# Kernel tuning notes

Measured on AMD Instinct MI355X. Metric: run time of the kernel, lower is better.

Reference implementation:

```python
import jax, jax.numpy as jnp
import numpy as np

NUM_EMBEDDINGS = 4096
EMBEDDING_DIM = 512
N_TOKENS = 32768
COMMITMENT_COST = 0.25


def setup_inputs() -> dict:
    key = jax.random.key(0)
    k1, k2 = jax.random.split(key)
    flat_input = jax.random.normal(k1, (N_TOKENS, EMBEDDING_DIM), dtype=jnp.float32)
    # torch init: uniform(-1/K, 1/K)
    weight = jax.random.uniform(k2, (NUM_EMBEDDINGS, EMBEDDING_DIM), dtype=jnp.float32,
                                minval=-1.0 / NUM_EMBEDDINGS, maxval=1.0 / NUM_EMBEDDINGS)
    return {"flat_input": flat_input, "weight": weight}


def reference(flat_input, weight):
    distances = (jnp.sum(flat_input ** 2, axis=1, keepdims=True)
                 + jnp.sum(weight ** 2, axis=1)
                 - 2.0 * jnp.matmul(flat_input, weight.T))
    encoding_indices = jnp.argmin(distances, axis=1)  # [N]
    # one-hot @ weight == direct gather of codebook rows
    quantized = weight[encoding_indices]  # [N, D]

    e_latent_loss = jnp.mean((jax.lax.stop_gradient(quantized) - flat_input) ** 2, axis=1)
    q_latent_loss = jnp.mean((quantized - jax.lax.stop_gradient(flat_input)) ** 2, axis=1)
    loss = q_latent_loss + COMMITMENT_COST * e_latent_loss  # [N]

    # straight-through estimator
    quantized_st = flat_input + jax.lax.stop_gradient(quantized - flat_input)

    # avg_probs = mean of one-hot encodings over batch = normalized code counts
    counts = jnp.zeros((NUM_EMBEDDINGS,), dtype=flat_input.dtype).at[encoding_indices].add(1.0)
    avg_probs = counts / flat_input.shape[0]
    perplexity = jnp.exp(-jnp.sum(avg_probs * jnp.log(avg_probs + 1e-10)))

    return quantized_st, loss, perplexity, encoding_indices
```

## Files before the change

kernel.cpp:

```cpp
#include <hip/hip_runtime.h>
#include <math.h>

#define N_TOK 32768
#define K_CODES 4096
#define DIM 512
#define COMMIT 0.25f
#define NCAND 8
#define NSPLIT 2
#define SPLIT_CODES (K_CODES / NSPLIT)
#define NITER (SPLIT_CODES / 256)
#define BIAS 0.125f

typedef short s16x8 __attribute__((ext_vector_type(8)));
typedef float f32x4 __attribute__((ext_vector_type(4)));
typedef unsigned int uint32;
typedef unsigned long long u64;
typedef unsigned short u16;

__device__ __forceinline__ u16 f2bf(float f) {
    uint32 b = __float_as_uint(f);
    return (u16)((b + 0x7FFFu + ((b >> 16) & 1u)) >> 16);
}

__device__ __forceinline__ void gload16(const u16* g, u16* l) {
    __builtin_amdgcn_global_load_lds(
        (const __attribute__((address_space(1))) void*)g,
        (__attribute__((address_space(3))) void*)l,
        16, 0, 0);
}

__global__ __launch_bounds__(256) void tobf16_kernel(const float* __restrict__ src,
                                                     u16* __restrict__ dst, int n4) {
    int i = blockIdx.x * 256 + threadIdx.x;
    int stride = gridDim.x * 256;
    for (; i < n4; i += stride) {
        float4 v = ((const float4*)src)[i];
        ushort4 o;
        o.x = f2bf(v.x); o.y = f2bf(v.y); o.z = f2bf(v.z); o.w = f2bf(v.w);
        ((ushort4*)dst)[i] = o;
    }
}

__global__ __launch_bounds__(256) void rowsq_np_kernel(const float* __restrict__ a,
                                                       float* __restrict__ out,
                                                       int nrows) {
    #pragma clang fp contract(off)
    const int gw   = (blockIdx.x * 256 + threadIdx.x) >> 6;
    const int lane = threadIdx.x & 63;
    const int row  = gw * 8 + (lane >> 3);
    const int j    = lane & 7;
    if (row >= nrows) return;
    const float* p = a + (size_t)row * DIM;
    float blk[4];
    #pragma unroll
    for (int b = 0; b < 4; ++b) {
        const float* q = p + b * 128;
        float v = q[j];
        float r = v * v;
        for (int i = 8; i < 128; i += 8) { float u = q[i + j]; r += u * u; }
        float s1 = r  + __shfl_xor(r, 1);
        float s2 = s1 + __shfl_xor(s1, 2);
        float s3 = s2 + __shfl_xor(s2, 4);
        blk[b] = s3;
    }
    float res = (blk[0] + blk[1]) + (blk[2] + blk[3]);
    if (j == 0) out[row] = res;
}

__global__ __launch_bounds__(512, 2) void screen_kernel(const u16* __restrict__ xb,
                                                        const u16* __restrict__ wb,
                                                        const float* __restrict__ w2f,
                                                        u64* __restrict__ candPart) {
    __shared__ __attribute__((aligned(16))) u16 POOL[49152];

    const int tid  = threadIdx.x;
    const int wv   = tid >> 6;
    const int wt   = wv >> 2;
    const int wc   = wv & 3;
    const int lane = tid & 63;
    const int quad = lane >> 4;
    const int n15  = lane & 15;
    const int m0   = blockIdx.x * 128;
    const int sbase = blockIdx.y * SPLIT_CODES;

    const int l8  = lane >> 3;
    const int qsw = (lane & 7) ^ l8;

    const u16* xg0 = xb + (size_t)(m0 + wv * 16 + 0 + l8) * DIM + qsw * 8;
    const u16* xg1 = xb + (size_t)(m0 + wv * 16 + 8 + l8) * DIM + qsw * 8;
    const size_t wofs0 = (size_t)(wv * 32 + 0  + l8) * DIM;
    const size_t wofs1 = (size_t)(wv * 32 + 8  + l8) * DIM;
    const size_t wofs2 = (size_t)(wv * 32 + 16 + l8) * DIM;
    const size_t wofs3 = (size_t)(wv * 32 + 24 + l8) * DIM;

    u16* ldsx0 = &POOL[0     + wv * 1024];
    u16* ldsx1 = &POOL[8192  + wv * 1024];
    u16* ldsw0 = &POOL[16384 + wv * 2048];
    u16* ldsw1 = &POOL[32768 + wv * 2048];

    uint32 r1[16], r2[16];
    #pragma unroll
    for (int i = 0; i < 16; ++i) { r1[i] = 0xFFFFFFFFu; r2[i] = 0xFFFFFFFFu; }

    const u16* wit = wb + (size_t)sbase * DIM + qsw * 8;

    {
        gload16(xg0, ldsx0);
        gload16(xg0 + 512, ldsx0 + 512);
    }
    gload16(xg1, ldsx0 + 512);
    gload16(wit + wofs0, ldsw0);
    gload16(wit + wofs1, ldsw0 + 512);
    gload16(wit + wofs2, ldsw0 + 1024);
    gload16(wit + wofs3, ldsw0 + 1536);
    __syncthreads();

    for (int it = 0; it < NITER; ++it) {
        const int nbase = sbase + it * 256;

        float w2pb[4];
        #pragma unroll
        for (int c = 0; c < 4; ++c) w2pb[c] = w2f[nbase + wc * 64 + c * 16 + n15] + BIAS;

        f32x4 acc[4][4];
        #pragma unroll
        for (int i = 0; i < 4; ++i)
            #pragma unroll
            for (int c = 0; c < 4; ++c) acc[i][c] = (f32x4){0.f, 0.f, 0.f, 0.f};

        for (int kc = 0; kc < 8; ++kc) {
            if (kc < 7) {
                const int nb = (kc + 1) & 1;
                u16* lx = nb ? ldsx1 : ldsx0;
                u16* lw = nb ? ldsw1 : ldsw0;
                const int ko = (kc + 1) * 64;
                gload16(xg0 + ko, lx);
                gload16(xg1 + ko, lx + 512);
                gload16(wit + wofs0 + ko, lw);
                gload16(wit + wofs1 + ko, lw + 512);
                gload16(wit + wofs2 + ko, lw + 1024);
                gload16(wit + wofs3 + ko, lw + 1536);
            } else if (it < NITER - 1) {
                const u16* wn = wit + (size_t)256 * DIM;
                gload16(xg0, ldsx0);
                gload16(xg1, ldsx0 + 512);
                gload16(wn + wofs0, ldsw0);
                gload16(wn + wofs1, ldsw0 + 512);
                gload16(wn + wofs2, ldsw0 + 1024);
                gload16(wn + wofs3, ldsw0 + 1536);
            }

            const u16* X = &POOL[(kc & 1) * 8192];
            const u16* W = &POOL[16384 + (kc & 1) * 16384];
            #pragma unroll
            for (int s = 0; s < 2; ++s) {
                const int lq = s * 4 + quad;
                s16x8 af[4], bf[4];
                #pragma unroll
                for (int i = 0; i < 4; ++i) {
                    const int tr = wt * 64 + i * 16 + n15;
                    af[i] = *(const s16x8*)&X[tr * 64 + (lq ^ (tr & 7)) * 8];
                }
                #pragma unroll
                for (int c = 0; c < 4; ++c) {
                    const int cr = wc * 64 + c * 16 + n15;
                    bf[c] = *(const s16x8*)&W[cr * 64 + (lq ^ (cr & 7)) * 8];
                }
                #pragma unroll
                for (int i = 0; i < 4; ++i)
                    #pragma unroll
                    for (int c = 0; c < 4; ++c)
                        acc[i][c] = __builtin_amdgcn_mfma_f32_16x16x32_bf16(af[i], bf[c], acc[i][c], 0, 0, 0);
            }
            __syncthreads();
        }

        #pragma unroll
        for (int i = 0; i < 4; ++i)
            #pragma unroll
            for (int r = 0; r < 4; ++r) {
                const int ti = i * 4 + r;
                #pragma unroll
                for (int c = 0; c < 4; ++c) {
                    float s = fmaf(-2.0f, acc[i][c][r], w2pb[c]);
                    uint32 key = (__float_as_uint(s) & 0xFFFFFFC0u) | (uint32)((it << 2) | c);
                    uint32 mx = r1[ti] > key ? r1[ti] : key;
                    r1[ti] = r1[ti] < key ? r1[ti] : key;
                    r2[ti] = r2[ti] < mx ? r2[ti] : mx;
                }
            }
        wit += (size_t)256 * DIM;
    }

    u64* MS = (u64*)POOL;
    for (int phase = 0; phase < 2; ++phase) {
        __syncthreads();
        if (wt == phase) {
            #pragma unroll
            for (int ti = 0; ti < 16; ++ti) {
                const int i = ti >> 2, r = ti & 3;
                const int tloc = i * 16 + quad * 4 + r;
                #pragma unroll
                for (int e = 0; e < 2; ++e) {
                    uint32 k  = e ? r2[ti] : r1[ti];
                    uint32 vb = k & 0xFFFFFFC0u;
                    uint32 id = k & 63u;
                    uint32 code = (uint32)(sbase + (id >> 2) * 256 + wc * 64 + (id & 3) * 16 + n15);
                    MS[tloc * 128 + (wc * 16 + n15) * 2 + e] = ((u64)vb << 32) | code;
                }
            }
        }
        __syncthreads();
        if (tid < 64) {
            u64 best[6];
            #pragma unroll
            for (int c = 0; c < 6; ++c) best[c] = 0xFFFFFFFFFFFFFFFFull;
            for (int e = 0; e < 128; ++e) {
                u64 v = MS[tid * 128 + e];
                if (v < best[5]) {
                    best[5] = v;
                    #pragma unroll
                    for (int p = 5; p > 0; --p)
                        if (best[p] < best[p - 1]) { u64 tv = best[p]; best[p] = best[p - 1]; best[p - 1] = tv; }
                }
            }
            const int token = m0 + phase * 64 + tid;
            u64* dst = candPart + ((size_t)blockIdx.y * N_TOK + token) * 6;
            #pragma unroll
            for (int c = 0; c < 6; ++c) dst[c] = best[c];
        }
    }
}

__global__ __launch_bounds__(256) void mergecand_kernel(const u64* __restrict__ candPart,
                                                        int* __restrict__ candF) {
    int t = blockIdx.x * 256 + threadIdx.x;
    u64 best[NCAND];
    #pragma unroll
    for (int c = 0; c < NCAND; ++c) best[c] = 0xFFFFFFFFFFFFFFFFull;
    for (int s = 0; s < NSPLIT; ++s) {
        const u64* src = candPart + ((size_t)s * N_TOK + t) * 6;
        #pragma unroll
        for (int c = 0; c < 6; ++c) {
            u64 v = src[c];
            if (v < best[NCAND - 1]) {
                best[NCAND - 1] = v;
                #pragma unroll
                for (int p = NCAND - 1; p > 0; --p)
                    if (best[p] < best[p - 1]) { u64 tv = best[p]; best[p] = best[p - 1]; best[p - 1] = tv; }
            }
        }
    }
    #pragma unroll
    for (int c = 0; c < NCAND; ++c) candF[(size_t)t * NCAND + c] = (int)(best[c] & 0xFFFu);
}

__global__ __launch_bounds__(256) void refine_kernel(const float* __restrict__ x,
                                                     const float* __restrict__ w,
                                                     const float* __restrict__ x2np,
                                                     const float* __restrict__ w2np,
                                                     const int* __restrict__ cand,
                                                     int* __restrict__ idx) {
    const int t    = blockIdx.x * 4 + (threadIdx.x >> 6);
    const int lane = threadIdx.x & 63;

    const float* xr = x + (size_t)t * DIM;
    float xv[8];
    #pragma unroll
    for (int j = 0; j < 8; ++j) xv[j] = xr[lane + 64 * j];
    const float x2 = x2np[t];

    float bd = 3.4e38f;
    int   bk = 0x7fffffff;
    for (int c = 0; c < NCAND; ++c) {
        int k = cand[(size_t)t * NCAND + c];
        const float* wr = w + (size_t)k * DIM;
        double m = 0.0;
        #pragma unroll
        for (int j = 0; j < 8; ++j)
            m = fma((double)xv[j], (double)wr[lane + 64 * j], m);
        #pragma unroll
        for (int off = 32; off >= 1; off >>= 1) m += __shfl_down(m, off);
        if (lane == 0) {
            #pragma clang fp contract(off)
            float m32 = (float)m;
            float T1  = x2 + w2np[k];
            float d   = T1 - 2.0f * m32;
            if (d < bd || (d == bd && k < bk)) { bd = d; bk = k; }
        }
    }
    if (lane == 0) idx[t] = bk;
}

__global__ __launch_bounds__(256) void gather_kernel(const float* __restrict__ x,
                                                     const float* __restrict__ w,
                                                     const int* __restrict__ idx,
                                                     float* __restrict__ out_q,
                                                     float* __restrict__ out_loss,
                                                     float* __restrict__ out_ind,
                                                     int* __restrict__ counts) {
    const int wave = threadIdx.x >> 6;
    const int lane = threadIdx.x & 63;
    const int token = blockIdx.x * 4 + wave;
    const int k = idx[token];

    const float4* xr = (const float4*)(x + (size_t)token * DIM);
    const float4* wr = (const float4*)(w + (size_t)k * DIM);
    float4*       qo = (float4*)(out_q + (size_t)token * DIM);

    float ss = 0.f;
    #pragma unroll
    for (int j = 0; j < 2; ++j) {
        int e = lane + j * 64;
        float4 xv = xr[e];
        float4 wv = wr[e];
        float4 d, o;
        d.x = wv.x - xv.x; o.x = xv.x + d.x;
        d.y = wv.y - xv.y; o.y = xv.y + d.y;
        d.z = wv.z - xv.z; o.z = xv.z + d.z;
        d.w = wv.w - xv.w; o.w = xv.w + d.w;
        ss += d.x * d.x + d.y * d.y + d.z * d.z + d.w * d.w;
        qo[e] = o;
    }
    #pragma unroll
    for (int off = 32; off >= 1; off >>= 1) ss += __shfl_down(ss, off);
    if (lane == 0) {
        float lm = ss * (1.0f / DIM);
        out_loss[token] = lm + COMMIT * lm;
        out_ind[token] = (float)k;
        atomicAdd(&counts[k], 1);
    }
}

__global__ __launch_bounds__(256) void perplex_kernel(const int* __restrict__ counts,
                                                      float* __restrict__ out2) {
    __shared__ double red[4];
    const int tid = threadIdx.x;
    const int lane = tid & 63;
    const int wid = tid >> 6;
    double s = 0.0;
    for (int t = tid; t < K_CODES; t += 256) {
        int c = counts[t];
        if (c) {
            double p = (double)c * (1.0 / N_TOK);
            s += p * log(p + 1e-10);
        }
    }
    #pragma unroll
    for (int off = 32; off >= 1; off >>= 1) s += __shfl_down(s, off);
    if (lane == 0) red[wid] = s;
    __syncthreads();
    if (tid == 0) {
        double t = red[0] + red[1] + red[2] + red[3];
        out2[0] = (float)exp(-t);
    }
}

extern "C" void kernel_launch(void* const* d_in, const int* in_sizes, int n_in,
                              void* d_out, int out_size, void* d_ws, size_t ws_size,
                              hipStream_t stream) {
    const float* x = (const float*)d_in[0];
    const float* w = (const float*)d_in[1];

    float* out0 = (float*)d_out;
    float* out1 = out0 + (size_t)N_TOK * DIM;
    float* out2 = out1 + N_TOK;
    float* out3 = out2 + 1;

    u64*   candPart = (u64*)d_ws;
    float* x2np     = (float*)(candPart + (size_t)NSPLIT * N_TOK * 6);
    float* w2np     = x2np + N_TOK;
    int*   idx      = (int*)(w2np + K_CODES);
    int*   counts   = idx + N_TOK;
    int*   candF    = counts + K_CODES;
    u16*   x_bf     = (u16*)(candF + (size_t)N_TOK * NCAND);
    u16*   w_bf     = x_bf + (size_t)N_TOK * DIM;

    hipMemsetAsync(counts, 0, K_CODES * sizeof(int), stream);

    tobf16_kernel<<<4096, 256, 0, stream>>>(x, x_bf, N_TOK * DIM / 4);
    tobf16_kernel<<<2048, 256, 0, stream>>>(w, w_bf, K_CODES * DIM / 4);
    rowsq_np_kernel<<<N_TOK / 32, 256, 0, stream>>>(x, x2np, N_TOK);
    rowsq_np_kernel<<<K_CODES / 32, 256, 0, stream>>>(w, w2np, K_CODES);
    screen_kernel<<<dim3(N_TOK / 128, NSPLIT), 512, 0, stream>>>(x_bf, w_bf, w2np, candPart);
    mergecand_kernel<<<N_TOK / 256, 256, 0, stream>>>(candPart, candF);
    refine_kernel<<<N_TOK / 4, 256, 0, stream>>>(x, w, x2np, w2np, candF, idx);
    gather_kernel<<<N_TOK / 4, 256, 0, stream>>>(x, w, idx, out0, out1, out3, counts);
    perplex_kernel<<<1, 256, 0, stream>>>(counts, out2);
}
```

Baseline: 433.6 us.

## Halve K-chunk to 32 and shrink LDS to raise screen-kernel occupancy

The screen kernel's K chunk per pipeline stage drops from 64 to 32 bf16 elements, which halves the double-buffered LDS pool from 96KB to 64KB. The launch-bounds hint goes from 2 to 4 blocks per CU. Global-to-LDS loads and the XOR swizzle are rewritten for 32-wide rows, and there are now 16 K-steps per tile instead of 8. The aim is more resident waves to hide memory latency, at the cost of twice as many __syncthreads barriers per tile and tighter register limits that may cause spills.

```diff
diff --git a/kernel.cpp b/kernel.cpp
--- a/kernel.cpp
+++ b/kernel.cpp
@@ -67,11 +67,11 @@
     if (j == 0) out[row] = res;
 }
 
-__global__ __launch_bounds__(512, 2) void screen_kernel(const u16* __restrict__ xb,
+__global__ __launch_bounds__(512, 4) void screen_kernel(const u16* __restrict__ xb,
                                                         const u16* __restrict__ wb,
                                                         const float* __restrict__ w2f,
                                                         u64* __restrict__ candPart) {
-    __shared__ __attribute__((aligned(16))) u16 POOL[49152];
+    __shared__ __attribute__((aligned(16))) u16 POOL[32768];
 
     const int tid  = threadIdx.x;
     const int wv   = tid >> 6;
@@ -83,20 +83,17 @@
     const int m0   = blockIdx.x * 128;
     const int sbase = blockIdx.y * SPLIT_CODES;
 
-    const int l8  = lane >> 3;
-    const int qsw = (lane & 7) ^ l8;
-
-    const u16* xg0 = xb + (size_t)(m0 + wv * 16 + 0 + l8) * DIM + qsw * 8;
-    const u16* xg1 = xb + (size_t)(m0 + wv * 16 + 8 + l8) * DIM + qsw * 8;
-    const size_t wofs0 = (size_t)(wv * 32 + 0  + l8) * DIM;
-    const size_t wofs1 = (size_t)(wv * 32 + 8  + l8) * DIM;
-    const size_t wofs2 = (size_t)(wv * 32 + 16 + l8) * DIM;
-    const size_t wofs3 = (size_t)(wv * 32 + 24 + l8) * DIM;
-
-    u16* ldsx0 = &POOL[0     + wv * 1024];
-    u16* ldsx1 = &POOL[8192  + wv * 1024];
-    u16* ldsw0 = &POOL[16384 + wv * 2048];
-    u16* ldsw1 = &POOL[32768 + wv * 2048];
+    const int l16 = lane >> 2;
+    const int qsw = (lane & 3) ^ (l16 & 3);
+
+    const u16* xg0 = xb + (size_t)(m0 + wv * 16 + l16) * DIM + qsw * 8;
+    const size_t wofs0 = (size_t)(wv * 32 + 0  + l16) * DIM;
+    const size_t wofs1 = (size_t)(wv * 32 + 16 + l16) * DIM;
+
+    u16* ldsx0 = &POOL[0    + wv * 512];
+    u16* ldsx1 = &POOL[4096 + wv * 512];
+    u16* ldsw0 = &POOL[8192  + wv * 1024];
+    u16* ldsw1 = &POOL[16384 + wv * 1024];
 
     uint32 r1[16], r2[16];
     #pragma unroll
@@ -104,15 +101,11 @@
 
     const u16* wit = wb + (size_t)sbase * DIM + qsw * 8;
 
-    {
-        gload16(xg0, ldsx0);
-        gload16(xg0 + 512, ldsx0 + 512);
-    }
-    gload16(xg1, ldsx0 + 512);
+    const int qx = (quad ^ (n15 & 3)) * 8;
+
+    gload16(xg0, ldsx0);
     gload16(wit + wofs0, ldsw0);
     gload16(wit + wofs1, ldsw0 + 512);
-    gload16(wit + wofs2, ldsw0 + 1024);
-    gload16(wit + wofs3, ldsw0 + 1536);
     __syncthreads();
 
     for (int it = 0; it < NITER; ++it) {
@@ -128,50 +121,40 @@
             #pragma unroll
             for (int c = 0; c < 4; ++c) acc[i][c] = (f32x4){0.f, 0.f, 0.f, 0.f};
 
-        for (int kc = 0; kc < 8; ++kc) {
-            if (kc < 7) {
+        for (int kc = 0; kc < 16; ++kc) {
+            if (kc < 15) {
                 const int nb = (kc + 1) & 1;
-                u16* lx = nb ? ldsx1 : ldsx0;
+                const int ko = (kc + 1) * 32;
+                gload16(xg0 + ko, nb ? ldsx1 : ldsx0);
                 u16* lw = nb ? ldsw1 : ldsw0;
-                const int ko = (kc + 1) * 64;
-                gload16(xg0 + ko, lx);
-                gload16(xg1 + ko, lx + 512);
                 gload16(wit + wofs0 + ko, lw);
                 gload16(wit + wofs1 + ko, lw + 512);
-                gload16(wit + wofs2 + ko, lw + 1024);
-                gload16(wit + wofs3 + ko, lw + 1536);
             } else if (it < NITER - 1) {
                 const u16* wn = wit + (size_t)256 * DIM;
                 gload16(xg0, ldsx0);
-                gload16(xg1, ldsx0 + 512);
                 gload16(wn + wofs0, ldsw0);
                 gload16(wn + wofs1, ldsw0 + 512);
-                gload16(wn + wofs2, ldsw0 + 1024);
-                gload16(wn + wofs3, ldsw0 + 1536);
-            }
-
-            const u16* X = &POOL[(kc & 1) * 8192];
-            const u16* W = &POOL[16384 + (kc & 1) * 16384];
-            #pragma unroll
-            for (int s = 0; s < 2; ++s) {
-                const int lq = s * 4 + quad;
-                s16x8 af[4], bf[4];
+            }
+
+            const u16* X = &POOL[(kc & 1) * 4096];
+            const u16* W = &POOL[8192 + (kc & 1) * 8192];
+            s16x8 af[4], bf[4];
+            #pragma unroll
+            for (int i = 0; i < 4; ++i) {
+                const int tr = wt * 64 + i * 16 + n15;
+                af[i] = *(const s16x8*)&X[tr * 32 + qx];
+            }
+            #pragma unroll
+            for (int c = 0; c < 4; ++c) {
+                const int cr = wc * 64 + c * 16 + n15;
+                bf[c] = *(const s16x8*)&W[cr * 32 + qx];
+            }
+            #pragma unroll
+            for (int i = 0; i < 4; ++i)
                 #pragma unroll
-                for (int i = 0; i < 4; ++i) {
-                    const int tr = wt * 64 + i * 16 + n15;
-                    af[i] = *(const s16x8*)&X[tr * 64 + (lq ^ (tr & 7)) * 8];
-                }
-                #pragma unroll
-                for (int c = 0; c < 4; ++c) {
-                    const int cr = wc * 64 + c * 16 + n15;
-                    bf[c] = *(const s16x8*)&W[cr * 64 + (lq ^ (cr & 7)) * 8];
-                }
-                #pragma unroll
-                for (int i = 0; i < 4; ++i)
-                    #pragma unroll
-                    for (int c = 0; c < 4; ++c)
-                        acc[i][c] = __builtin_amdgcn_mfma_f32_16x16x32_bf16(af[i], bf[c], acc[i][c], 0, 0, 0);
-            }
+                for (int c = 0; c < 4; ++c)
+                    acc[i][c] = __builtin_amdgcn_mfma_f32_16x16x32_bf16(af[i], bf[c], acc[i][c], 0, 0, 0);
+
             __syncthreads();
         }
 
```

Result: slower. 548.8 us (+26.6%).

## Triple-buffer LDS tiles with a flattened loop and vmcnt-based single barrier

Applied to the files above, without the earlier changes.

Replaces the double-buffered nested loop (one __syncthreads per k-chunk plus a stall at each codebook tile boundary) with a flattened 64-step loop over three LDS buffers. It prefetches two steps ahead, uses s_waitcnt vmcnt plus a single raw barrier per step, and keeps loads streaming across codebook tile boundaries. The w2 norms for the split are staged once into LDS instead of being read from global memory every tile. LDS use rises to about 152 KB per block, which may limit occupancy below the launch-bounds target of 2 blocks per CU.

```diff
diff --git a/kernel.cpp b/kernel.cpp
--- a/kernel.cpp
+++ b/kernel.cpp
@@ -71,7 +71,7 @@
                                                         const u16* __restrict__ wb,
                                                         const float* __restrict__ w2f,
                                                         u64* __restrict__ candPart) {
-    __shared__ __attribute__((aligned(16))) u16 POOL[49152];
+    __shared__ __attribute__((aligned(16))) u16 POOL[77824];
 
     const int tid  = threadIdx.x;
     const int wv   = tid >> 6;
@@ -86,72 +86,65 @@
     const int l8  = lane >> 3;
     const int qsw = (lane & 7) ^ l8;
 
-    const u16* xg0 = xb + (size_t)(m0 + wv * 16 + 0 + l8) * DIM + qsw * 8;
-    const u16* xg1 = xb + (size_t)(m0 + wv * 16 + 8 + l8) * DIM + qsw * 8;
-    const size_t wofs0 = (size_t)(wv * 32 + 0  + l8) * DIM;
-    const size_t wofs1 = (size_t)(wv * 32 + 8  + l8) * DIM;
-    const size_t wofs2 = (size_t)(wv * 32 + 16 + l8) * DIM;
-    const size_t wofs3 = (size_t)(wv * 32 + 24 + l8) * DIM;
-
-    u16* ldsx0 = &POOL[0     + wv * 1024];
-    u16* ldsx1 = &POOL[8192  + wv * 1024];
-    u16* ldsw0 = &POOL[16384 + wv * 2048];
-    u16* ldsw1 = &POOL[32768 + wv * 2048];
+    const u16* xg0 = xb + (size_t)(m0 + wv * 16 + l8) * DIM + qsw * 8;
+    const u16* xg1 = xg0 + (size_t)8 * DIM;
+    const u16* wg0 = wb + (size_t)(sbase + wv * 32 + 0  + l8) * DIM + qsw * 8;
+    const u16* wg1 = wg0 + (size_t)8 * DIM;
+    const u16* wg2 = wg0 + (size_t)16 * DIM;
+    const u16* wg3 = wg0 + (size_t)24 * DIM;
+
+    {
+        float* w2l = (float*)&POOL[73728];
+        for (int i = tid; i < SPLIT_CODES; i += 512)
+            w2l[i] = w2f[sbase + i] + BIAS;
+    }
 
     uint32 r1[16], r2[16];
     #pragma unroll
     for (int i = 0; i < 16; ++i) { r1[i] = 0xFFFFFFFFu; r2[i] = 0xFFFFFFFFu; }
 
-    const u16* wit = wb + (size_t)sbase * DIM + qsw * 8;
-
-    {
-        gload16(xg0, ldsx0);
-        gload16(xg0 + 512, ldsx0 + 512);
-    }
-    gload16(xg1, ldsx0 + 512);
-    gload16(wit + wofs0, ldsw0);
-    gload16(wit + wofs1, ldsw0 + 512);
-    gload16(wit + wofs2, ldsw0 + 1024);
-    gload16(wit + wofs3, ldsw0 + 1536);
+    f32x4 acc[4][4];
+    #pragma unroll
+    for (int i = 0; i < 4; ++i)
+        #pragma unroll
+        for (int c = 0; c < 4; ++c) acc[i][c] = (f32x4){0.f, 0.f, 0.f, 0.f};
+
+    #pragma unroll
+    for (int tt = 0; tt < 2; ++tt) {
+        const int ko = tt * 64;
+        gload16(xg0 + ko, &POOL[tt * 8192 + wv * 1024]);
+        gload16(xg1 + ko, &POOL[tt * 8192 + wv * 1024 + 512]);
+        gload16(wg0 + ko, &POOL[24576 + tt * 16384 + wv * 2048]);
+        gload16(wg1 + ko, &POOL[24576 + tt * 16384 + wv * 2048 + 512]);
+        gload16(wg2 + ko, &POOL[24576 + tt * 16384 + wv * 2048 + 1024]);
+        gload16(wg3 + ko, &POOL[24576 + tt * 16384 + wv * 2048 + 1536]);
+    }
     __syncthreads();
 
-    for (int it = 0; it < NITER; ++it) {
-        const int nbase = sbase + it * 256;
-
-        float w2pb[4];
-        #pragma unroll
-        for (int c = 0; c < 4; ++c) w2pb[c] = w2f[nbase + wc * 64 + c * 16 + n15] + BIAS;
-
-        f32x4 acc[4][4];
-        #pragma unroll
-        for (int i = 0; i < 4; ++i)
-            #pragma unroll
-            for (int c = 0; c < 4; ++c) acc[i][c] = (f32x4){0.f, 0.f, 0.f, 0.f};
-
-        for (int kc = 0; kc < 8; ++kc) {
-            if (kc < 7) {
-                const int nb = (kc + 1) & 1;
-                u16* lx = nb ? ldsx1 : ldsx0;
-                u16* lw = nb ? ldsw1 : ldsw0;
-                const int ko = (kc + 1) * 64;
-                gload16(xg0 + ko, lx);
-                gload16(xg1 + ko, lx + 512);
-                gload16(wit + wofs0 + ko, lw);
-                gload16(wit + wofs1 + ko, lw + 512);
-                gload16(wit + wofs2 + ko, lw + 1024);
-                gload16(wit + wofs3 + ko, lw + 1536);
-            } else if (it < NITER - 1) {
-                const u16* wn = wit + (size_t)256 * DIM;
-                gload16(xg0, ldsx0);
-                gload16(xg1, ldsx0 + 512);
-                gload16(wn + wofs0, ldsw0);
-                gload16(wn + wofs1, ldsw0 + 512);
-                gload16(wn + wofs2, ldsw0 + 1024);
-                gload16(wn + wofs3, ldsw0 + 1536);
-            }
-
-            const u16* X = &POOL[(kc & 1) * 8192];
-            const u16* W = &POOL[16384 + (kc & 1) * 16384];
+    int bufc = 0;
+    for (int t = 0; t < 64; ++t) {
+        if (t < 63) asm volatile("s_waitcnt vmcnt(6)" ::: "memory");
+        else        asm volatile("s_waitcnt vmcnt(0)" ::: "memory");
+        __builtin_amdgcn_s_barrier();
+        __builtin_amdgcn_sched_barrier(0);
+
+        if (t <= 61) {
+            const int bn  = (bufc == 0) ? 2 : bufc - 1;
+            const int tn  = t + 2;
+            const size_t co = (size_t)(tn >> 3) * (256 * DIM) + (tn & 7) * 64;
+            const int ko  = (tn & 7) * 64;
+            const size_t xo = (size_t)ko;
+            gload16(xg0 + xo, &POOL[bn * 8192 + wv * 1024]);
+            gload16(xg1 + xo, &POOL[bn * 8192 + wv * 1024 + 512]);
+            gload16(wg0 + co, &POOL[24576 + bn * 16384 + wv * 2048]);
+            gload16(wg1 + co, &POOL[24576 + bn * 16384 + wv * 2048 + 512]);
+            gload16(wg2 + co, &POOL[24576 + bn * 16384 + wv * 2048 + 1024]);
+            gload16(wg3 + co, &POOL[24576 + bn * 16384 + wv * 2048 + 1536]);
+        }
+
+        {
+            const u16* X = &POOL[bufc * 8192];
+            const u16* W = &POOL[24576 + bufc * 16384];
             #pragma unroll
             for (int s = 0; s < 2; ++s) {
                 const int lq = s * 4 + quad;
@@ -172,24 +165,36 @@
                     for (int c = 0; c < 4; ++c)
                         acc[i][c] = __builtin_amdgcn_mfma_f32_16x16x32_bf16(af[i], bf[c], acc[i][c], 0, 0, 0);
             }
-            __syncthreads();
-        }
-
-        #pragma unroll
-        for (int i = 0; i < 4; ++i)
-            #pragma unroll
-            for (int r = 0; r < 4; ++r) {
-                const int ti = i * 4 + r;
-                #pragma unroll
-                for (int c = 0; c < 4; ++c) {
-                    float s = fmaf(-2.0f, acc[i][c][r], w2pb[c]);
-                    uint32 key = (__float_as_uint(s) & 0xFFFFFFC0u) | (uint32)((it << 2) | c);
-                    uint32 mx = r1[ti] > key ? r1[ti] : key;
-                    r1[ti] = r1[ti] < key ? r1[ti] : key;
-                    r2[ti] = r2[ti] < mx ? r2[ti] : mx;
-                }
-            }
-        wit += (size_t)256 * DIM;
+        }
+
+        if ((t & 7) == 7) {
+            const int it = t >> 3;
+            const float* w2l = (const float*)&POOL[73728];
+            float w2pb[4];
+            #pragma unroll
+            for (int c = 0; c < 4; ++c)
+                w2pb[c] = w2l[it * 256 + wc * 64 + c * 16 + n15];
+            #pragma unroll
+            for (int i = 0; i < 4; ++i)
+                #pragma unroll
+                for (int r = 0; r < 4; ++r) {
+                    const int ti = i * 4 + r;
+                    #pragma unroll
+                    for (int c = 0; c < 4; ++c) {
+                        float s = fmaf(-2.0f, acc[i][c][r], w2pb[c]);
+                        uint32 key = (__float_as_uint(s) & 0xFFFFFFC0u) | (uint32)((it << 2) | c);
+                        uint32 mx = r1[ti] > key ? r1[ti] : key;
+                        r1[ti] = r1[ti] < key ? r1[ti] : key;
+                        r2[ti] = r2[ti] < mx ? r2[ti] : mx;
+                    }
+                }
+            #pragma unroll
+            for (int i = 0; i < 4; ++i)
+                #pragma unroll
+                for (int c = 0; c < 4; ++c) acc[i][c] = (f32x4){0.f, 0.f, 0.f, 0.f};
+        }
+
+        bufc = (bufc == 2) ? 0 : bufc + 1;
     }
 
     u64* MS = (u64*)POOL;
```

Result: slower. 446.9 us (+3.1%).
